# Performance work log

Hardware: AMD Instinct MI355X
Metric: run time of the kernel (lower is better)

Reference implementation:

```python
import jax, jax.numpy as jnp
import numpy as np

B, T, H = 32, 2048, 1024

def setup_inputs() -> dict:
    key = jax.random.key(0)
    k1, k2, k3 = jax.random.split(key, 3)
    hidden = jax.random.normal(k1, (B, H), dtype=jnp.float32)
    encoder_outputs = jax.random.normal(k2, (B, T, H), dtype=jnp.float32)
    W = jax.random.normal(k3, (H, H), dtype=jnp.float32) / np.sqrt(H)
    return {"hidden": hidden, "encoder_outputs": encoder_outputs, "W": W}

def reference(hidden, encoder_outputs, W):
    # Linear (no bias): torch nn.Linear applies x @ W.T
    encoder_transformed = jnp.einsum('bth,oh->bto', encoder_outputs, W)
    # score: [B, T] = bmm([B,T,H], [B,H,1]).squeeze
    score = jnp.einsum('bth,bh->bt', encoder_transformed, hidden)
    attention_weights = jax.nn.softmax(score, axis=1)
    # context: [B, H]
    context_vector = jnp.einsum('bt,bth->bh', attention_weights, encoder_outputs)
    return (context_vector, attention_weights)
```

## Files before the change

kernel.cpp:

```cpp
#include <hip/hip_runtime.h>

#define B 32
#define T 2048
#define H 1024

__global__ __launch_bounds__(256) void compute_v_kernel(
    const float* __restrict__ hidden, const float* __restrict__ W,
    float* __restrict__ v) {
  const int b = blockIdx.y;
  const int og = threadIdx.x >> 6;
  const int hl = threadIdx.x & 63;
  const int h = blockIdx.x * 64 + hl;
  __shared__ float sh[H];
  __shared__ float red[4][64];
  for (int i = threadIdx.x; i < H; i += 256) sh[i] = hidden[b * H + i];
  __syncthreads();
  float acc[8] = {0.f, 0.f, 0.f, 0.f, 0.f, 0.f, 0.f, 0.f};
  const int ob = og * 256;
  for (int oo = 0; oo < 256; oo += 8) {
#pragma unroll
    for (int k = 0; k < 8; ++k) {
      const int o = ob + oo + k;
      acc[k] = fmaf(sh[o], W[(size_t)o * H + h], acc[k]);
    }
  }
  float a = ((acc[0] + acc[1]) + (acc[2] + acc[3])) +
            ((acc[4] + acc[5]) + (acc[6] + acc[7]));
  red[og][hl] = a;
  __syncthreads();
  if (og == 0)
    v[b * H + h] = (red[0][hl] + red[1][hl]) + (red[2][hl] + red[3][hl]);
}

__global__ __launch_bounds__(256) void scores_kernel(
    const float* __restrict__ enc, const float* __restrict__ v,
    float* __restrict__ score) {
  const int b = blockIdx.y;
  const int wave = threadIdx.x >> 6;
  const int lane = threadIdx.x & 63;
  const float4* v4 = (const float4*)(v + b * H);
  float4 vr[4];
#pragma unroll
  for (int j = 0; j < 4; ++j) vr[j] = v4[j * 64 + lane];
  const int t0 = blockIdx.x * 64 + wave * 16;
  for (int it = 0; it < 16; it += 2) {
    const int ta = t0 + it, tb = t0 + it + 1;
    const float4* ea4 = (const float4*)(enc + ((size_t)b * T + ta) * H);
    const float4* eb4 = (const float4*)(enc + ((size_t)b * T + tb) * H);
    float4 ea[4], eb[4];
#pragma unroll
    for (int j = 0; j < 4; ++j) ea[j] = ea4[j * 64 + lane];
#pragma unroll
    for (int j = 0; j < 4; ++j) eb[j] = eb4[j * 64 + lane];
    float accA = 0.f, accB = 0.f;
#pragma unroll
    for (int j = 0; j < 4; ++j) {
      accA += ea[j].x * vr[j].x + ea[j].y * vr[j].y + ea[j].z * vr[j].z +
              ea[j].w * vr[j].w;
      accB += eb[j].x * vr[j].x + eb[j].y * vr[j].y + eb[j].z * vr[j].z +
              eb[j].w * vr[j].w;
    }
#pragma unroll
    for (int off = 32; off; off >>= 1) {
      accA += __shfl_down(accA, off, 64);
      accB += __shfl_down(accB, off, 64);
    }
    if (lane == 0) {
      score[b * T + ta] = accA;
      score[b * T + tb] = accB;
    }
  }
}

__global__ __launch_bounds__(256) void softmax_stats_kernel(
    const float* __restrict__ score, float2* __restrict__ stats) {
  const int b = blockIdx.x;
  const int tid = threadIdx.x;
  const int wave = tid >> 6;
  const int lane = tid & 63;
  __shared__ float red[4];
  const float* row = score + b * T;

  float x[8];
  float m = -1e30f;
#pragma unroll
  for (int j = 0; j < 8; ++j) {
    x[j] = row[j * 256 + tid];
    m = fmaxf(m, x[j]);
  }
#pragma unroll
  for (int off = 32; off; off >>= 1) m = fmaxf(m, __shfl_down(m, off, 64));
  if (lane == 0) red[wave] = m;
  __syncthreads();
  m = fmaxf(fmaxf(red[0], red[1]), fmaxf(red[2], red[3]));
  __syncthreads();

  float s = 0.f;
#pragma unroll
  for (int j = 0; j < 8; ++j) s += __expf(x[j] - m);
#pragma unroll
  for (int off = 32; off; off >>= 1) s += __shfl_down(s, off, 64);
  if (lane == 0) red[wave] = s;
  __syncthreads();
  if (tid == 0) {
    const float total = (red[0] + red[1]) + (red[2] + red[3]);
    stats[b] = make_float2(m, 1.f / total);
  }
}

#define TCH 64
#define NCH (T / TCH)
__global__ __launch_bounds__(256) void context_partial_kernel(
    const float* __restrict__ enc, float* __restrict__ attn,
    const float2* __restrict__ stats, float* __restrict__ partial) {
  const int b = blockIdx.y;
  const int c = blockIdx.x;
  const int tid = threadIdx.x;
  __shared__ float wa[TCH];
  const float2 st = stats[b];
  if (tid < TCH) {
    const float raw = attn[b * T + c * TCH + tid];
    const float w = __expf(raw - st.x) * st.y;
    attn[b * T + c * TCH + tid] = w;
    wa[tid] = w;
  }
  __syncthreads();
  float4 a0 = {0, 0, 0, 0}, a1 = {0, 0, 0, 0}, a2 = {0, 0, 0, 0},
         a3 = {0, 0, 0, 0};
  const float4* base = (const float4*)(enc + ((size_t)b * T + c * TCH) * H);
  for (int t = 0; t < TCH; t += 4) {
    float4 e0 = base[(size_t)(t + 0) * (H / 4) + tid];
    float4 e1 = base[(size_t)(t + 1) * (H / 4) + tid];
    float4 e2 = base[(size_t)(t + 2) * (H / 4) + tid];
    float4 e3 = base[(size_t)(t + 3) * (H / 4) + tid];
    const float w0 = wa[t], w1 = wa[t + 1], w2 = wa[t + 2], w3 = wa[t + 3];
    a0.x = fmaf(w0, e0.x, a0.x); a0.y = fmaf(w0, e0.y, a0.y);
    a0.z = fmaf(w0, e0.z, a0.z); a0.w = fmaf(w0, e0.w, a0.w);
    a1.x = fmaf(w1, e1.x, a1.x); a1.y = fmaf(w1, e1.y, a1.y);
    a1.z = fmaf(w1, e1.z, a1.z); a1.w = fmaf(w1, e1.w, a1.w);
    a2.x = fmaf(w2, e2.x, a2.x); a2.y = fmaf(w2, e2.y, a2.y);
    a2.z = fmaf(w2, e2.z, a2.z); a2.w = fmaf(w2, e2.w, a2.w);
    a3.x = fmaf(w3, e3.x, a3.x); a3.y = fmaf(w3, e3.y, a3.y);
    a3.z = fmaf(w3, e3.z, a3.z); a3.w = fmaf(w3, e3.w, a3.w);
  }
  float4 r;
  r.x = (a0.x + a1.x) + (a2.x + a3.x);
  r.y = (a0.y + a1.y) + (a2.y + a3.y);
  r.z = (a0.z + a1.z) + (a2.z + a3.z);
  r.w = (a0.w + a1.w) + (a2.w + a3.w);
  ((float4*)(partial + ((size_t)b * NCH + c) * H))[tid] = r;
}

__global__ __launch_bounds__(256) void context_reduce_kernel(
    const float* __restrict__ partial, float* __restrict__ ctx) {
  const int b = blockIdx.x;
  const int tid = threadIdx.x;
  float4 acc = {0, 0, 0, 0};
  const float4* p = (const float4*)(partial + (size_t)b * NCH * H);
#pragma unroll 8
  for (int c = 0; c < NCH; ++c) {
    float4 e = p[c * (H / 4) + tid];
    acc.x += e.x; acc.y += e.y; acc.z += e.z; acc.w += e.w;
  }
  ((float4*)(ctx + b * H))[tid] = acc;
}

extern "C" void kernel_launch(void* const* d_in, const int* in_sizes, int n_in,
                              void* d_out, int out_size, void* d_ws,
                              size_t ws_size, hipStream_t stream) {
  const float* hidden = (const float*)d_in[0];
  const float* enc = (const float*)d_in[1];
  const float* W = (const float*)d_in[2];

  float* out = (float*)d_out;
  float* out_ctx = out;
  float* out_attn = out + B * H;

  float* v = (float*)d_ws;
  float* partial = v + B * H;
  float2* stats = (float2*)(partial + B * NCH * H);

  compute_v_kernel<<<dim3(H / 64, B), 256, 0, stream>>>(hidden, W, v);
  scores_kernel<<<dim3(T / 64, B), 256, 0, stream>>>(enc, v, out_attn);
  softmax_stats_kernel<<<B, 256, 0, stream>>>(out_attn, stats);
  context_partial_kernel<<<dim3(NCH, B), 256, 0, stream>>>(enc, out_attn, stats,
                                                           partial);
  context_reduce_kernel<<<B, 256, 0, stream>>>(partial, out_ctx);
}
```

Before: 424.5 us.

## Fuse context reduction via atomics, reverse block order, deepen load batching

Drops the separate context reduce kernel and its partial buffer. Each context block now atomically adds its partial sum into the output, which is zeroed inside the v kernel. Context blocks are visited in reverse order so the tail of the encoder tensor, the part most likely still in cache after the scores pass, is read first. The scores kernel handles four rows per iteration with one vectorised store, and the context loop loads eight rows per iteration. In exchange the result carries atomic contention and a summation order that is no longer deterministic.

```diff
diff --git a/kernel.cpp b/kernel.cpp
--- a/kernel.cpp
+++ b/kernel.cpp
@@ -6,13 +6,16 @@
 
 __global__ __launch_bounds__(256) void compute_v_kernel(
     const float* __restrict__ hidden, const float* __restrict__ W,
-    float* __restrict__ v) {
+    float* __restrict__ v, float* __restrict__ ctx) {
   const int b = blockIdx.y;
   const int og = threadIdx.x >> 6;
   const int hl = threadIdx.x & 63;
   const int h = blockIdx.x * 64 + hl;
   __shared__ float sh[H];
   __shared__ float red[4][64];
+  if (blockIdx.x == 0) {
+    for (int i = threadIdx.x; i < H; i += 256) ctx[b * H + i] = 0.f;
+  }
   for (int i = threadIdx.x; i < H; i += 256) sh[i] = hidden[b * H + i];
   __syncthreads();
   float acc[8] = {0.f, 0.f, 0.f, 0.f, 0.f, 0.f, 0.f, 0.f};
@@ -42,33 +45,33 @@
   float4 vr[4];
 #pragma unroll
   for (int j = 0; j < 4; ++j) vr[j] = v4[j * 64 + lane];
+  const float4* ebase = (const float4*)(enc + (size_t)b * T * H);
   const int t0 = blockIdx.x * 64 + wave * 16;
-  for (int it = 0; it < 16; it += 2) {
-    const int ta = t0 + it, tb = t0 + it + 1;
-    const float4* ea4 = (const float4*)(enc + ((size_t)b * T + ta) * H);
-    const float4* eb4 = (const float4*)(enc + ((size_t)b * T + tb) * H);
-    float4 ea[4], eb[4];
+  for (int it = 0; it < 16; it += 4) {
+    const int t = t0 + it;
+    float4 e[4][4];
 #pragma unroll
-    for (int j = 0; j < 4; ++j) ea[j] = ea4[j * 64 + lane];
+    for (int r = 0; r < 4; ++r) {
+      const float4* ep = ebase + (size_t)(t + r) * (H / 4);
 #pragma unroll
-    for (int j = 0; j < 4; ++j) eb[j] = eb4[j * 64 + lane];
-    float accA = 0.f, accB = 0.f;
+      for (int j = 0; j < 4; ++j) e[r][j] = ep[j * 64 + lane];
+    }
+    float a[4] = {0.f, 0.f, 0.f, 0.f};
 #pragma unroll
-    for (int j = 0; j < 4; ++j) {
-      accA += ea[j].x * vr[j].x + ea[j].y * vr[j].y + ea[j].z * vr[j].z +
-              ea[j].w * vr[j].w;
-      accB += eb[j].x * vr[j].x + eb[j].y * vr[j].y + eb[j].z * vr[j].z +
-              eb[j].w * vr[j].w;
+    for (int r = 0; r < 4; ++r) {
+#pragma unroll
+      for (int j = 0; j < 4; ++j) {
+        a[r] += e[r][j].x * vr[j].x + e[r][j].y * vr[j].y +
+                e[r][j].z * vr[j].z + e[r][j].w * vr[j].w;
+      }
     }
 #pragma unroll
     for (int off = 32; off; off >>= 1) {
-      accA += __shfl_down(accA, off, 64);
-      accB += __shfl_down(accB, off, 64);
+#pragma unroll
+      for (int r = 0; r < 4; ++r) a[r] += __shfl_down(a[r], off, 64);
     }
-    if (lane == 0) {
-      score[b * T + ta] = accA;
-      score[b * T + tb] = accB;
-    }
+    if (lane == 0)
+      *(float4*)(score + b * T + t) = make_float4(a[0], a[1], a[2], a[3]);
   }
 }
 
@@ -110,11 +113,11 @@
 
 #define TCH 64
 #define NCH (T / TCH)
-__global__ __launch_bounds__(256) void context_partial_kernel(
+__global__ __launch_bounds__(256) void context_kernel(
     const float* __restrict__ enc, float* __restrict__ attn,
-    const float2* __restrict__ stats, float* __restrict__ partial) {
-  const int b = blockIdx.y;
-  const int c = blockIdx.x;
+    const float2* __restrict__ stats, float* __restrict__ ctx) {
+  const int b = (B - 1) - blockIdx.y;
+  const int c = (NCH - 1) - blockIdx.x;
   const int tid = threadIdx.x;
   __shared__ float wa[TCH];
   const float2 st = stats[b];
@@ -128,12 +131,18 @@
   float4 a0 = {0, 0, 0, 0}, a1 = {0, 0, 0, 0}, a2 = {0, 0, 0, 0},
          a3 = {0, 0, 0, 0};
   const float4* base = (const float4*)(enc + ((size_t)b * T + c * TCH) * H);
-  for (int t = 0; t < TCH; t += 4) {
+  for (int t = 0; t < TCH; t += 8) {
     float4 e0 = base[(size_t)(t + 0) * (H / 4) + tid];
     float4 e1 = base[(size_t)(t + 1) * (H / 4) + tid];
     float4 e2 = base[(size_t)(t + 2) * (H / 4) + tid];
     float4 e3 = base[(size_t)(t + 3) * (H / 4) + tid];
-    const float w0 = wa[t], w1 = wa[t + 1], w2 = wa[t + 2], w3 = wa[t + 3];
+    float4 e4 = base[(size_t)(t + 4) * (H / 4) + tid];
+    float4 e5 = base[(size_t)(t + 5) * (H / 4) + tid];
+    float4 e6 = base[(size_t)(t + 6) * (H / 4) + tid];
+    float4 e7 = base[(size_t)(t + 7) * (H / 4) + tid];
+    const float w0 = wa[t + 0], w1 = wa[t + 1], w2 = wa[t + 2],
+                w3 = wa[t + 3], w4 = wa[t + 4], w5 = wa[t + 5],
+                w6 = wa[t + 6], w7 = wa[t + 7];
     a0.x = fmaf(w0, e0.x, a0.x); a0.y = fmaf(w0, e0.y, a0.y);
     a0.z = fmaf(w0, e0.z, a0.z); a0.w = fmaf(w0, e0.w, a0.w);
     a1.x = fmaf(w1, e1.x, a1.x); a1.y = fmaf(w1, e1.y, a1.y);
@@ -142,27 +151,25 @@
     a2.z = fmaf(w2, e2.z, a2.z); a2.w = fmaf(w2, e2.w, a2.w);
     a3.x = fmaf(w3, e3.x, a3.x); a3.y = fmaf(w3, e3.y, a3.y);
     a3.z = fmaf(w3, e3.z, a3.z); a3.w = fmaf(w3, e3.w, a3.w);
+    a0.x = fmaf(w4, e4.x, a0.x); a0.y = fmaf(w4, e4.y, a0.y);
+    a0.z = fmaf(w4, e4.z, a0.z); a0.w = fmaf(w4, e4.w, a0.w);
+    a1.x = fmaf(w5, e5.x, a1.x); a1.y = fmaf(w5, e5.y, a1.y);
+    a1.z = fmaf(w5, e5.z, a1.z); a1.w = fmaf(w5, e5.w, a1.w);
+    a2.x = fmaf(w6, e6.x, a2.x); a2.y = fmaf(w6, e6.y, a2.y);
+    a2.z = fmaf(w6, e6.z, a2.z); a2.w = fmaf(w6, e6.w, a2.w);
+    a3.x = fmaf(w7, e7.x, a3.x); a3.y = fmaf(w7, e7.y, a3.y);
+    a3.z = fmaf(w7, e7.z, a3.z); a3.w = fmaf(w7, e7.w, a3.w);
   }
   float4 r;
   r.x = (a0.x + a1.x) + (a2.x + a3.x);
   r.y = (a0.y + a1.y) + (a2.y + a3.y);
   r.z = (a0.z + a1.z) + (a2.z + a3.z);
   r.w = (a0.w + a1.w) + (a2.w + a3.w);
-  ((float4*)(partial + ((size_t)b * NCH + c) * H))[tid] = r;
-}
-
-__global__ __launch_bounds__(256) void context_reduce_kernel(
-    const float* __restrict__ partial, float* __restrict__ ctx) {
-  const int b = blockIdx.x;
-  const int tid = threadIdx.x;
-  float4 acc = {0, 0, 0, 0};
-  const float4* p = (const float4*)(partial + (size_t)b * NCH * H);
-#pragma unroll 8
-  for (int c = 0; c < NCH; ++c) {
-    float4 e = p[c * (H / 4) + tid];
-    acc.x += e.x; acc.y += e.y; acc.z += e.z; acc.w += e.w;
-  }
-  ((float4*)(ctx + b * H))[tid] = acc;
+  float* dst = ctx + (size_t)b * H + tid * 4;
+  atomicAdd(dst + 0, r.x);
+  atomicAdd(dst + 1, r.y);
+  atomicAdd(dst + 2, r.z);
+  atomicAdd(dst + 3, r.w);
 }
 
 extern "C" void kernel_launch(void* const* d_in, const int* in_sizes, int n_in,
@@ -177,13 +184,11 @@
   float* out_attn = out + B * H;
 
   float* v = (float*)d_ws;
-  float* partial = v + B * H;
-  float2* stats = (float2*)(partial + B * NCH * H);
+  float2* stats = (float2*)(v + B * H);
 
-  compute_v_kernel<<<dim3(H / 64, B), 256, 0, stream>>>(hidden, W, v);
+  compute_v_kernel<<<dim3(H / 64, B), 256, 0, stream>>>(hidden, W, v, out_ctx);
   scores_kernel<<<dim3(T / 64, B), 256, 0, stream>>>(enc, v, out_attn);
   softmax_stats_kernel<<<B, 256, 0, stream>>>(out_attn, stats);
-  context_partial_kernel<<<dim3(NCH, B), 256, 0, stream>>>(enc, out_attn, stats,
-                                                           partial);
-  context_reduce_kernel<<<B, 256, 0, stream>>>(partial, out_ctx);
+  context_kernel<<<dim3(NCH, B), 256, 0, stream>>>(enc, out_attn, stats,
+                                                   out_ctx);
 }
```

Result: no change. 424.3 us (-0.0%).
